# Kernel tuning notes

Measured on AMD Instinct MI355X. Metric: run time of the kernel, lower is better.

The kernel has to match this reference:

```python
import jax, jax.numpy as jnp
import numpy as np
from jax.scipy.special import erfinv

EMBED = 384
HEADS = 6
HEAD_DIM = EMBED // HEADS  # 64
N_FREQS = HEAD_DIM // 2    # 32
SEQ = 1025                 # 1 CLS + 32*32 patches
POS_DIM = 2
MIN_FREQ, MAX_FREQ = 0.1, 1000.0


def _phi(m: int) -> float:
    x = 2.0
    for _ in range(10):
        x = (1.0 + x) ** (1.0 / (m + 1.0))
    return x


def _uniform_directions(n: int, d: int) -> jnp.ndarray:
    # golden-ratio quasi-random directions, normalized (matches uniform_directions_jax)
    g = _phi(d)
    alpha = (1.0 / g) ** jnp.arange(1, d + 1, dtype=jnp.float32)
    i = jnp.arange(1, n + 1, dtype=jnp.float32)[:, None]
    z = jnp.fmod(i * alpha, 1.0)
    dirs = erfinv(2.0 * z - 1.0)
    return dirs / jnp.linalg.norm(dirs, axis=1, keepdims=True)


def _rope_freqs() -> jnp.ndarray:  # [h, F, P]
    omega = MIN_FREQ * (MAX_FREQ / MIN_FREQ) ** jnp.linspace(0.0, 1.0, N_FREQS)
    dirs = _uniform_directions(HEADS * N_FREQS, POS_DIM).reshape(HEADS, N_FREQS, POS_DIM)
    return dirs * omega.reshape(1, N_FREQS, 1)


def _coords_2d() -> jnp.ndarray:  # [S, 2], CLS at origin, patches in [-1,1]^2
    n = int(np.sqrt(SEQ - 1))  # 32
    yy, xx = jnp.meshgrid(jnp.arange(n), jnp.arange(n), indexing='ij')
    xf = xx.flatten().astype(jnp.float32) / (n - 1) * 2 - 1
    yf = yy.flatten().astype(jnp.float32) / (n - 1) * 2 - 1
    patch = jnp.stack([xf, yf], axis=1)
    return jnp.concatenate([jnp.zeros((1, 2), jnp.float32), patch], axis=0)


def _apply_rope(t_bshd, freqs_hFP, coords_SP):
    # theta: [S, h, F]
    theta = jnp.einsum('hfp,sp->shf', freqs_hFP, coords_SP)
    cos, sin = jnp.cos(theta), jnp.sin(theta)  # broadcast over batch
    x1, y1 = jnp.split(t_bshd, 2, axis=-1)     # [b,s,h,F] each
    return jnp.concatenate([x1 * cos - y1 * sin, x1 * sin + y1 * cos], axis=-1)


def setup_inputs() -> dict:
    key = jax.random.key(0)
    ks = jax.random.split(key, 6)
    scale = 1.0 / np.sqrt(EMBED)
    return {
        'x':  jax.random.normal(ks[0], (16, SEQ, EMBED), jnp.float32),
        'Wq': jax.random.normal(ks[1], (EMBED, EMBED), jnp.float32) * scale,
        'Wk': jax.random.normal(ks[2], (EMBED, EMBED), jnp.float32) * scale,
        'Wv': jax.random.normal(ks[3], (EMBED, EMBED), jnp.float32) * scale,
        'Wo': jax.random.normal(ks[4], (EMBED, EMBED), jnp.float32) * scale,
        'bo': jnp.zeros((EMBED,), jnp.float32),
    }


def reference(x, Wq, Wk, Wv, Wo, bo):
    b, s, e = x.shape
    freqs = _rope_freqs()   # constant buffers
    coords = _coords_2d()
    q = (x @ Wq).reshape(b, s, HEADS, HEAD_DIM)
    k = (x @ Wk).reshape(b, s, HEADS, HEAD_DIM)
    v = (x @ Wv).reshape(b, s, HEADS, HEAD_DIM)
    q = _apply_rope(q, freqs, coords)
    k = _apply_rope(k, freqs, coords)
    scores = jnp.einsum('blhd,bmhd->bhlm', q, k) / np.sqrt(HEAD_DIM)
    attn = jax.nn.softmax(scores, axis=-1)
    out = jnp.einsum('bhlm,bmhd->blhd', attn, v).reshape(b, s, e)
    return out @ Wo + bo
```

## Files before the change

kernel.cpp:

```cpp
#include <hip/hip_runtime.h>
#include <hip/hip_bf16.h>
#include <math.h>

#define EMBED 384
#define HEADS 6
#define HD    64
#define NF    32
#define SEQ   1025
#define SEQP  1088
#define BATCH 16
#define MTOT  (BATCH*SEQ)
#define NCHUNK 17
#define LSTRIDE 72
#define VSTR   68

#define NB_X2B 6150
#define NB_TW  144
#define NB_RT  769

typedef __bf16 bf16x8 __attribute__((ext_vector_type(8)));
typedef __bf16 bf16x4 __attribute__((ext_vector_type(4)));
typedef float  f32x4  __attribute__((ext_vector_type(4)));
typedef short  s16x4  __attribute__((ext_vector_type(4)));

#define MFMA_BF16(A,B,C) __builtin_amdgcn_mfma_f32_16x16x32_bf16((A),(B),(C),0,0,0)
#define MFMA16(A,B,C) __builtin_amdgcn_mfma_f32_16x16x16bf16_1k((A),(B),(C),0,0,0)

#define GLL16(gp, lp) __builtin_amdgcn_global_load_lds( \
    (const __attribute__((address_space(1))) void*)(gp), \
    (__attribute__((address_space(3))) void*)(lp), 16, 0, 0)

__device__ __forceinline__ __bf16 f2bf(float f){
    __hip_bfloat16 h = __float2bfloat16(f);
    return *reinterpret_cast<__bf16*>(&h);
}
__device__ __forceinline__ short bfbits(float f){
    __hip_bfloat16 h = __float2bfloat16(f);
    return *reinterpret_cast<short*>(&h);
}

__device__ __forceinline__ float erfinv_f(float x){
    float w = -log1pf(-x*x);
    float p;
    if (w < 5.0f){
        w -= 2.5f;
        p = 2.81022636e-08f;
        p = fmaf(p, w, 3.43273939e-07f);
        p = fmaf(p, w, -3.5233877e-06f);
        p = fmaf(p, w, -4.39150654e-06f);
        p = fmaf(p, w, 0.00021858087f);
        p = fmaf(p, w, -0.00125372503f);
        p = fmaf(p, w, -0.00417768164f);
        p = fmaf(p, w, 0.246640727f);
        p = fmaf(p, w, 1.50140941f);
    } else {
        w = sqrtf(w) - 3.0f;
        p = -0.000200214257f;
        p = fmaf(p, w, 0.000100950558f);
        p = fmaf(p, w, 0.00134934322f);
        p = fmaf(p, w, -0.00367342844f);
        p = fmaf(p, w, 0.00573950773f);
        p = fmaf(p, w, -0.0076224613f);
        p = fmaf(p, w, 0.00943887047f);
        p = fmaf(p, w, 1.00167406f);
        p = fmaf(p, w, 2.83297682f);
    }
    return p * x;
}

__global__ __launch_bounds__(256) void prep_kernel(
    const float* __restrict__ x, __hip_bfloat16* __restrict__ xb,
    const float* __restrict__ Wq, const float* __restrict__ Wk,
    const float* __restrict__ Wv, const float* __restrict__ Wo,
    __hip_bfloat16* __restrict__ Wt,
    float* __restrict__ cos_t, float* __restrict__ sin_t)
{
    __shared__ float tile[64][65];
    const int bid = blockIdx.x;
    const int tid = threadIdx.x;

    if (bid < NB_X2B){
        int i = bid*256 + tid;
        float4 v = *reinterpret_cast<const float4*>(x + (size_t)i*4);
        bf16x4 b; b[0]=f2bf(v.x); b[1]=f2bf(v.y); b[2]=f2bf(v.z); b[3]=f2bf(v.w);
        *reinterpret_cast<bf16x4*>(reinterpret_cast<__bf16*>(xb) + (size_t)i*4) = b;
        return;
    }
    if (bid < NB_X2B + NB_TW){
        int idx = bid - NB_X2B;
        const int mat = idx / 36;
        const int rem = idx % 36;
        const int kx = rem / 6, ny = rem % 6;
        const float* W = (mat==0)?Wq:(mat==1)?Wk:(mat==2)?Wv:Wo;
        const int k0 = kx*64, n0 = ny*64;
        const int c = tid & 63, rq = tid >> 6;
        #pragma unroll
        for (int i = 0; i < 16; ++i){
            int row = rq*16 + i;
            tile[row][c] = W[(size_t)(k0+row)*EMBED + n0 + c];
        }
        __syncthreads();
        #pragma unroll
        for (int i = 0; i < 16; ++i){
            int nr = rq*16 + i;
            Wt[((size_t)mat*EMBED + n0 + nr)*EMBED + k0 + c] = __float2bfloat16(tile[c][nr]);
        }
        return;
    }
    int idx = (bid - NB_X2B - NB_TW)*256 + tid;
    if (idx >= SEQ*HEADS*NF) return;
    int f  = idx & (NF-1);
    int hf = idx / NF;
    int h  = hf % HEADS;
    int s  = hf / HEADS;

    double xd = 2.0;
    #pragma unroll
    for (int it = 0; it < 10; ++it) xd = cbrt(1.0 + xd);
    float a1 = (float)(1.0 / xd);
    float a2 = a1 * a1;

    float fi = (float)(h*NF + f + 1);
    float z1 = fmodf(fi * a1, 1.0f);
    float z2 = fmodf(fi * a2, 1.0f);
    float d1 = erfinv_f(2.0f*z1 - 1.0f);
    float d2 = erfinv_f(2.0f*z2 - 1.0f);
    float inv = 1.0f / sqrtf(d1*d1 + d2*d2);
    d1 *= inv; d2 *= inv;

    float omega = 0.1f * powf(10000.0f, (float)f / 31.0f);
    float fx = d1 * omega, fy = d2 * omega;

    float cx = 0.0f, cy = 0.0f;
    if (s > 0){
        int pi = s - 1;
        cx = (float)(pi & 31) / 31.0f * 2.0f - 1.0f;
        cy = (float)(pi >> 5) / 31.0f * 2.0f - 1.0f;
    }
    float theta = fx*cx + fy*cy;
    float sv, cv;
    sincosf(theta, &sv, &cv);
    cos_t[idx] = cv;
    sin_t[idx] = sv;
}

__global__ __launch_bounds__(256, 3) void qkv_rope_kernel(
    const __hip_bfloat16* __restrict__ xb_,
    const __hip_bfloat16* __restrict__ Wt,
    const float* __restrict__ cos_t,
    const float* __restrict__ sin_t,
    __hip_bfloat16* __restrict__ qbuf,
    __hip_bfloat16* __restrict__ kbuf,
    __hip_bfloat16* __restrict__ vbuf)
{
    __shared__ __align__(16) __bf16 xs[2][128*32];
    __shared__ __align__(16) __bf16 bt[2][128*32];
    const int tid = threadIdx.x;
    const int m0 = blockIdx.x * 128;
    const int j  = blockIdx.y;
    const __bf16* xb = reinterpret_cast<const __bf16*>(xb_);
    const __bf16* wt = reinterpret_cast<const __bf16*>(Wt);

    const int w = tid >> 6;
    const int lane = tid & 63;
    const int quad = lane >> 4, low = lane & 15;
    const int rg = lane >> 2, cg = lane & 3;

    int arow[2], brow[2], loff[2];
    #pragma unroll
    for (int i = 0; i < 2; ++i){
        int row = (w*2 + i)*16 + rg;
        int am = m0 + row; if (am > MTOT-1) am = MTOT-1;
        arow[i] = am;
        brow[i] = j*128 + row;
        loff[i] = (w*2 + i)*1024;
    }

    #pragma unroll
    for (int i = 0; i < 2; ++i){
        GLL16(xb + (size_t)arow[i]*EMBED + cg*8, (char*)xs[0] + loff[i]);
        GLL16(wt + (size_t)brow[i]*EMBED + cg*8, (char*)bt[0] + loff[i]);
    }
    __syncthreads();

    const int mh = w >> 1, nh = w & 1;
    const int mw0 = m0 + mh*64;

    f32x4 acc[4][4] = {};
    for (int kb = 0; kb < 12; ++kb){
        const int cur = kb & 1;
        if (kb < 11){
            const int k1 = (kb+1)*32;
            #pragma unroll
            for (int i = 0; i < 2; ++i){
                GLL16(xb + (size_t)arow[i]*EMBED + k1 + cg*8, (char*)xs[cur^1] + loff[i]);
                GLL16(wt + (size_t)brow[i]*EMBED + k1 + cg*8, (char*)bt[cur^1] + loff[i]);
            }
        }
        bf16x8 af[4], bfr[4];
        #pragma unroll
        for (int mt = 0; mt < 4; ++mt)
            af[mt] = *reinterpret_cast<const bf16x8*>(&xs[cur][(mh*64 + mt*16 + low)*32 + quad*8]);
        #pragma unroll
        for (int t = 0; t < 4; ++t)
            bfr[t] = *reinterpret_cast<const bf16x8*>(&bt[cur][(nh*64 + t*16 + low)*32 + quad*8]);
        #pragma unroll
        for (int t = 0; t < 4; ++t)
            #pragma unroll
            for (int mt = 0; mt < 4; ++mt)
                acc[mt][t] = MFMA_BF16(af[mt], bfr[t], acc[mt][t]);
        if (kb < 11) __syncthreads();
    }

    const int n64 = j*2 + nh;
    const int mat = n64 / 6;
    const int h   = n64 % 6;

    if (mat == 2){
        #pragma unroll
        for (int mt = 0; mt < 4; ++mt)
            #pragma unroll
            for (int t = 0; t < 4; ++t)
                #pragma unroll
                for (int r = 0; r < 4; ++r){
                    int m = mw0 + mt*16 + quad*4 + r;
                    if (m < MTOT){
                        int b = m / SEQ, s = m % SEQ;
                        vbuf[((size_t)(b*HEADS + h)*SEQ + s)*HD + t*16 + low] = __float2bfloat16(acc[mt][t][r]);
                    }
                }
    } else {
        __hip_bfloat16* ob = (mat == 0) ? qbuf : kbuf;
        const float qs_ = (mat == 0) ? 0.125f : 1.0f;
        #pragma unroll
        for (int mt = 0; mt < 4; ++mt)
            #pragma unroll
            for (int t = 0; t < 2; ++t)
                #pragma unroll
                for (int r = 0; r < 4; ++r){
                    int m = mw0 + mt*16 + quad*4 + r;
                    if (m < MTOT){
                        int b = m / SEQ, s = m % SEQ;
                        int f = t*16 + low;
                        float cv = cos_t[(s*HEADS + h)*NF + f];
                        float sv = sin_t[(s*HEADS + h)*NF + f];
                        float x1 = acc[mt][t][r];
                        float y1 = acc[mt][t+2][r];
                        size_t base = ((size_t)(b*HEADS + h)*SEQ + s)*HD;
                        ob[base + f]      = __float2bfloat16((x1*cv - y1*sv)*qs_);
                        ob[base + NF + f] = __float2bfloat16((x1*sv + y1*cv)*qs_);
                    }
                }
    }
}

__global__ __launch_bounds__(256) void vt_transpose_kernel(
    const __hip_bfloat16* __restrict__ v, __hip_bfloat16* __restrict__ vt)
{
    __shared__ __bf16 tileT[64*72];
    const int tid = threadIdx.x;
    const int bh = blockIdx.x;
    const int s0 = blockIdx.y * 64;
    const __bf16* vb = reinterpret_cast<const __bf16*>(v) + (size_t)bh*SEQ*HD;
    #pragma unroll
    for (int i = 0; i < 2; ++i){
        int ch = tid + i*256;
        int srow = ch >> 3, dg = ch & 7;
        int s = s0 + srow; if (s > SEQ-1) s = SEQ-1;
        bf16x8 val = *reinterpret_cast<const bf16x8*>(vb + (size_t)s*HD + dg*8);
        #pragma unroll
        for (int e = 0; e < 8; ++e)
            tileT[(dg*8 + e)*72 + srow] = val[e];
    }
    __syncthreads();
    __bf16* ot = reinterpret_cast<__bf16*>(vt) + (size_t)bh*HD*SEQP;
    #pragma unroll
    for (int i = 0; i < 2; ++i){
        int ch = tid + i*256;
        int d = ch >> 3, sg = ch & 7;
        bf16x8 val = *reinterpret_cast<const bf16x8*>(&tileT[d*72 + sg*8]);
        *reinterpret_cast<bf16x8*>(ot + (size_t)d*SEQP + s0 + sg*8) = val;
    }
}

__global__ __launch_bounds__(256, 4) void attn_kernel(
    const __hip_bfloat16* __restrict__ qbuf,
    const __hip_bfloat16* __restrict__ kbuf,
    const __hip_bfloat16* __restrict__ vtbuf,
    __hip_bfloat16* __restrict__ aout)
{
    __shared__ __align__(16) __bf16 kls[64*LSTRIDE];
    __shared__ __align__(16) __bf16 vls[64*VSTR];
    const int tid  = threadIdx.x;
    const int w    = tid >> 6;
    const int lane = tid & 63;
    const int quad = lane >> 4, low = lane & 15;
    const int id = blockIdx.x;
    const int bh = id % 96;
    const int qt = id / 96;
    const int b = bh / HEADS, h = bh % HEADS;
    const __bf16* qb = reinterpret_cast<const __bf16*>(qbuf);
    const __bf16* kb = reinterpret_cast<const __bf16*>(kbuf);
    const __bf16* vt = reinterpret_cast<const __bf16*>(vtbuf);
    const size_t base   = (size_t)bh * SEQ * HD;
    const size_t vtbase = (size_t)bh * HD * SEQP;
    const int q0 = qt*128 + w*32;

    int srow[2], sgk[2], soffk[2], soffv[2];
    #pragma unroll
    for (int i = 0; i < 2; ++i){
        int ch = tid + i*256;
        srow[i] = ch >> 3; sgk[i] = ch & 7;
        soffk[i] = srow[i]*LSTRIDE + sgk[i]*8;
        soffv[i] = srow[i]*VSTR    + sgk[i]*8;
    }

    bf16x8 bq[2][2];
    #pragma unroll
    for (int nt = 0; nt < 2; ++nt){
        int qs = q0 + nt*16 + low; if (qs > SEQ-1) qs = SEQ-1;
        #pragma unroll
        for (int ks = 0; ks < 2; ++ks)
            bq[nt][ks] = *reinterpret_cast<const bf16x8*>(qb + base + (size_t)qs*HD + ks*32 + quad*8);
    }

    bf16x8 kr[2], vr[2];
    #pragma unroll
    for (int i = 0; i < 2; ++i){
        int kk = srow[i]; if (kk > SEQ-1) kk = SEQ-1;
        kr[i] = *reinterpret_cast<const bf16x8*>(kb + base + (size_t)kk*HD + sgk[i]*8);
        vr[i] = *reinterpret_cast<const bf16x8*>(vt + vtbase + (size_t)srow[i]*SEQP + sgk[i]*8);
    }

    f32x4 o[2][4] = {};
    float l_i[2] = {0.f, 0.f};

    for (int c = 0; c < NCHUNK; ++c){
        const int c0 = c*64;
        __syncthreads();
        #pragma unroll
        for (int i = 0; i < 2; ++i){
            *reinterpret_cast<bf16x8*>(&kls[soffk[i]]) = kr[i];
            bf16x4 vlo = __builtin_shufflevector(vr[i], vr[i], 0,1,2,3);
            bf16x4 vhi = __builtin_shufflevector(vr[i], vr[i], 4,5,6,7);
            *reinterpret_cast<bf16x4*>(&vls[soffv[i]])     = vlo;
            *reinterpret_cast<bf16x4*>(&vls[soffv[i] + 4]) = vhi;
        }
        __syncthreads();
        if (c + 1 < NCHUNK){
            const int c1 = c0 + 64;
            #pragma unroll
            for (int i = 0; i < 2; ++i){
                int kk = c1 + srow[i]; if (kk > SEQ-1) kk = SEQ-1;
                kr[i] = *reinterpret_cast<const bf16x8*>(kb + base + (size_t)kk*HD + sgk[i]*8);
                vr[i] = *reinterpret_cast<const bf16x8*>(vt + vtbase + (size_t)srow[i]*SEQP + c1 + sgk[i]*8);
            }
        }
        f32x4 st[4][2] = {};
        #pragma unroll
        for (int kt = 0; kt < 4; ++kt)
            #pragma unroll
            for (int ks = 0; ks < 2; ++ks){
                bf16x8 ak = *reinterpret_cast<const bf16x8*>(&kls[(kt*16 + low)*LSTRIDE + ks*32 + quad*8]);
                #pragma unroll
                for (int nt = 0; nt < 2; ++nt)
                    st[kt][nt] = MFMA_BF16(ak, bq[nt][ks], st[kt][nt]);
            }
        if (c0 + 64 > SEQ){
            #pragma unroll
            for (int kt = 0; kt < 4; ++kt)
                #pragma unroll
                for (int r = 0; r < 4; ++r){
                    int key = c0 + kt*16 + quad*4 + r;
                    if (key >= SEQ){ st[kt][0][r] = -1e30f; st[kt][1][r] = -1e30f; }
                }
        }
        s16x4 pa[4][2];
        #pragma unroll
        for (int nt = 0; nt < 2; ++nt)
            #pragma unroll
            for (int kt = 0; kt < 4; ++kt)
                #pragma unroll
                for (int r = 0; r < 4; ++r){
                    float p = __expf(st[kt][nt][r]);
                    l_i[nt] += p;
                    pa[kt][nt][r] = bfbits(p);
                }
        #pragma unroll
        for (int kt = 0; kt < 4; ++kt)
            #pragma unroll
            for (int dt = 0; dt < 4; ++dt){
                const s16x4 bv = *reinterpret_cast<const s16x4*>(&vls[(dt*16 + low)*VSTR + kt*16 + quad*4]);
                #pragma unroll
                for (int nt = 0; nt < 2; ++nt)
                    o[nt][dt] = MFMA16(pa[kt][nt], bv, o[nt][dt]);
            }
    }

    #pragma unroll
    for (int nt = 0; nt < 2; ++nt){
        l_i[nt] += __shfl_xor(l_i[nt], 16, 64);
        l_i[nt] += __shfl_xor(l_i[nt], 32, 64);
    }
    float lq[2][4];
    #pragma unroll
    for (int nt = 0; nt < 2; ++nt)
        #pragma unroll
        for (int r = 0; r < 4; ++r)
            lq[nt][r] = __shfl(l_i[nt], quad*4 + r, 64);

    #pragma unroll
    for (int nt = 0; nt < 2; ++nt)
        #pragma unroll
        for (int r = 0; r < 4; ++r){
            int s = q0 + nt*16 + quad*4 + r;
            if (s < SEQ){
                float inv = 1.0f / lq[nt][r];
                __hip_bfloat16* dst = aout + ((size_t)b*SEQ + s)*EMBED + h*HD;
                #pragma unroll
                for (int dt = 0; dt < 4; ++dt)
                    dst[dt*16 + low] = __float2bfloat16(o[nt][dt][r]*inv);
            }
        }
}

__global__ __launch_bounds__(128) void outproj_kernel(
    const __hip_bfloat16* __restrict__ a,
    const __hip_bfloat16* __restrict__ Wt,
    const float* __restrict__ bo,
    float* __restrict__ out)
{
    __shared__ __align__(16) __bf16 xs[2][64*32];
    __shared__ __align__(16) __bf16 bt[2][128*32];
    const int tid = threadIdx.x;
    const int m0 = blockIdx.x * 64;
    const int j  = blockIdx.y;
    const __bf16* ab = reinterpret_cast<const __bf16*>(a);
    const __bf16* wt = reinterpret_cast<const __bf16*>(Wt) + (size_t)3*EMBED*EMBED;

    const int w = tid >> 6;
    const int lane = tid & 63;
    const int quad = lane >> 4, low = lane & 15;
    const int rg = lane >> 2, cg = lane & 3;

    int arow[2], aoff[2];
    #pragma unroll
    for (int i = 0; i < 2; ++i){
        int row = (w*2 + i)*16 + rg;
        int am = m0 + row; if (am > MTOT-1) am = MTOT-1;
        arow[i] = am;
        aoff[i] = (w*2 + i)*1024;
    }
    int brow[4], boff[4];
    #pragma unroll
    for (int i = 0; i < 4; ++i){
        int row = (w*4 + i)*16 + rg;
        brow[i] = j*128 + row;
        boff[i] = (w*4 + i)*1024;
    }

    #pragma unroll
    for (int i = 0; i < 2; ++i)
        GLL16(ab + (size_t)arow[i]*EMBED + cg*8, (char*)xs[0] + aoff[i]);
    #pragma unroll
    for (int i = 0; i < 4; ++i)
        GLL16(wt + (size_t)brow[i]*EMBED + cg*8, (char*)bt[0] + boff[i]);
    __syncthreads();

    f32x4 acc[4][4] = {};
    for (int kb = 0; kb < 12; ++kb){
        const int cur = kb & 1;
        if (kb < 11){
            const int k1 = (kb+1)*32;
            #pragma unroll
            for (int i = 0; i < 2; ++i)
                GLL16(ab + (size_t)arow[i]*EMBED + k1 + cg*8, (char*)xs[cur^1] + aoff[i]);
            #pragma unroll
            for (int i = 0; i < 4; ++i)
                GLL16(wt + (size_t)brow[i]*EMBED + k1 + cg*8, (char*)bt[cur^1] + boff[i]);
        }
        bf16x8 af[4], bfr[4];
        #pragma unroll
        for (int mt = 0; mt < 4; ++mt)
            af[mt] = *reinterpret_cast<const bf16x8*>(&xs[cur][(mt*16 + low)*32 + quad*8]);
        #pragma unroll
        for (int t = 0; t < 4; ++t)
            bfr[t] = *reinterpret_cast<const bf16x8*>(&bt[cur][(w*64 + t*16 + low)*32 + quad*8]);
        #pragma unroll
        for (int t = 0; t < 4; ++t)
            #pragma unroll
            for (int mt = 0; mt < 4; ++mt)
                acc[mt][t] = MFMA_BF16(af[mt], bfr[t], acc[mt][t]);
        if (kb < 11) __syncthreads();
    }

    #pragma unroll
    for (int t = 0; t < 4; ++t){
        const int n = j*128 + w*64 + t*16 + low;
        const float bias = bo[n];
        #pragma unroll
        for (int mt = 0; mt < 4; ++mt)
            #pragma unroll
            for (int r = 0; r < 4; ++r){
                const int m = m0 + mt*16 + quad*4 + r;
                if (m < MTOT) out[(size_t)m*EMBED + n] = acc[mt][t][r] + bias;
            }
    }
}

extern "C" void kernel_launch(void* const* d_in, const int* in_sizes, int n_in,
                              void* d_out, int out_size, void* d_ws, size_t ws_size,
                              hipStream_t stream)
{
    const float* x  = (const float*)d_in[0];
    const float* Wq = (const float*)d_in[1];
    const float* Wk = (const float*)d_in[2];
    const float* Wv = (const float*)d_in[3];
    const float* Wo = (const float*)d_in[4];
    const float* bo = (const float*)d_in[5];
    float* out = (float*)d_out;

    const size_t NE = (size_t)MTOT * EMBED;
    const size_t VT = (size_t)BATCH*HEADS*HD*SEQP;
    char* ws = (char*)d_ws;
    size_t off = 0;
    __hip_bfloat16* qbuf = (__hip_bfloat16*)(ws + off); off += 2*NE;
    __hip_bfloat16* kbuf = (__hip_bfloat16*)(ws + off); off += 2*NE;
    __hip_bfloat16* abuf = (__hip_bfloat16*)(ws + off); off += 2*NE;
    __hip_bfloat16* vbuf = (__hip_bfloat16*)(ws + off); off += 2*NE;
    __hip_bfloat16* xbuf = (__hip_bfloat16*)(ws + off); off += 2*NE;
    __hip_bfloat16* vt   = (__hip_bfloat16*)(ws + off); off += 2*VT;
    __hip_bfloat16* Wt   = (__hip_bfloat16*)(ws + off); off += (size_t)4*EMBED*EMBED*2;
    float* cos_t = (float*)(ws + off); off += (size_t)SEQ*HEADS*NF*4;
    float* sin_t = (float*)(ws + off); off += (size_t)SEQ*HEADS*NF*4;

    prep_kernel<<<dim3(NB_X2B + NB_TW + NB_RT), dim3(256), 0, stream>>>(
        x, xbuf, Wq, Wk, Wv, Wo, Wt, cos_t, sin_t);
    qkv_rope_kernel<<<dim3((MTOT + 127)/128, 9), dim3(256), 0, stream>>>(xbuf, Wt, cos_t, sin_t, qbuf, kbuf, vbuf);
    vt_transpose_kernel<<<dim3(96, 17), dim3(256), 0, stream>>>(vbuf, vt);
    attn_kernel<<<dim3(864), dim3(256), 0, stream>>>(qbuf, kbuf, vt, abuf);
    outproj_kernel<<<dim3((MTOT + 63)/64, 3), dim3(128), 0, stream>>>(abuf, Wt, bo, out);
}
```

Before: 206.2 us.

## Fuse V transpose into QKV GEMM epilogue and drop separate transpose kernel

```diff
diff --git a/kernel.cpp b/kernel.cpp
--- a/kernel.cpp
+++ b/kernel.cpp
@@ -13,10 +13,12 @@
 #define NCHUNK 17
 #define LSTRIDE 72
 #define VSTR   68
+#define TSTR   66
 
 #define NB_X2B 6150
 #define NB_TW  144
 #define NB_RT  769
+#define NB_VF  192
 
 typedef __bf16 bf16x8 __attribute__((ext_vector_type(8)));
 typedef __bf16 bf16x4 __attribute__((ext_vector_type(4)));
@@ -73,7 +75,8 @@
     const float* __restrict__ Wq, const float* __restrict__ Wk,
     const float* __restrict__ Wv, const float* __restrict__ Wo,
     __hip_bfloat16* __restrict__ Wt,
-    float* __restrict__ cos_t, float* __restrict__ sin_t)
+    float* __restrict__ cos_t, float* __restrict__ sin_t,
+    __hip_bfloat16* __restrict__ vt)
 {
     __shared__ float tile[64][65];
     const int bid = blockIdx.x;
@@ -107,41 +110,51 @@
         }
         return;
     }
-    int idx = (bid - NB_X2B - NB_TW)*256 + tid;
-    if (idx >= SEQ*HEADS*NF) return;
-    int f  = idx & (NF-1);
-    int hf = idx / NF;
-    int h  = hf % HEADS;
-    int s  = hf / HEADS;
-
-    double xd = 2.0;
-    #pragma unroll
-    for (int it = 0; it < 10; ++it) xd = cbrt(1.0 + xd);
-    float a1 = (float)(1.0 / xd);
-    float a2 = a1 * a1;
-
-    float fi = (float)(h*NF + f + 1);
-    float z1 = fmodf(fi * a1, 1.0f);
-    float z2 = fmodf(fi * a2, 1.0f);
-    float d1 = erfinv_f(2.0f*z1 - 1.0f);
-    float d2 = erfinv_f(2.0f*z2 - 1.0f);
-    float inv = 1.0f / sqrtf(d1*d1 + d2*d2);
-    d1 *= inv; d2 *= inv;
-
-    float omega = 0.1f * powf(10000.0f, (float)f / 31.0f);
-    float fx = d1 * omega, fy = d2 * omega;
-
-    float cx = 0.0f, cy = 0.0f;
-    if (s > 0){
-        int pi = s - 1;
-        cx = (float)(pi & 31) / 31.0f * 2.0f - 1.0f;
-        cy = (float)(pi >> 5) / 31.0f * 2.0f - 1.0f;
-    }
-    float theta = fx*cx + fy*cy;
-    float sv, cv;
-    sincosf(theta, &sv, &cv);
-    cos_t[idx] = cv;
-    sin_t[idx] = sv;
+    if (bid < NB_X2B + NB_TW + NB_RT){
+        int idx = (bid - NB_X2B - NB_TW)*256 + tid;
+        if (idx >= SEQ*HEADS*NF) return;
+        int f  = idx & (NF-1);
+        int hf = idx / NF;
+        int h  = hf % HEADS;
+        int s  = hf / HEADS;
+
+        double xd = 2.0;
+        #pragma unroll
+        for (int it = 0; it < 10; ++it) xd = cbrt(1.0 + xd);
+        float a1 = (float)(1.0 / xd);
+        float a2 = a1 * a1;
+
+        float fi = (float)(h*NF + f + 1);
+        float z1 = fmodf(fi * a1, 1.0f);
+        float z2 = fmodf(fi * a2, 1.0f);
+        float d1 = erfinv_f(2.0f*z1 - 1.0f);
+        float d2 = erfinv_f(2.0f*z2 - 1.0f);
+        float inv = 1.0f / sqrtf(d1*d1 + d2*d2);
+        d1 *= inv; d2 *= inv;
+
+        float omega = 0.1f * powf(10000.0f, (float)f / 31.0f);
+        float fx = d1 * omega, fy = d2 * omega;
+
+        float cx = 0.0f, cy = 0.0f;
+        if (s > 0){
+            int pi = s - 1;
+            cx = (float)(pi & 31) / 31.0f * 2.0f - 1.0f;
+            cy = (float)(pi >> 5) / 31.0f * 2.0f - 1.0f;
+        }
+        float theta = fx*cx + fy*cy;
+        float sv, cv;
+        sincosf(theta, &sv, &cv);
+        cos_t[idx] = cv;
+        sin_t[idx] = sv;
+        return;
+    }
+    {
+        int g = (bid - NB_X2B - NB_TW - NB_RT)*256 + tid;
+        int row = g >> 3, sg = g & 7;
+        bf16x8 z = {};
+        *reinterpret_cast<bf16x8*>(reinterpret_cast<__bf16*>(vt)
+            + (size_t)row*SEQP + 1024 + sg*8) = z;
+    }
 }
 
 __global__ __launch_bounds__(256, 3) void qkv_rope_kernel(
@@ -151,15 +164,15 @@
     const float* __restrict__ sin_t,
     __hip_bfloat16* __restrict__ qbuf,
     __hip_bfloat16* __restrict__ kbuf,
-    __hip_bfloat16* __restrict__ vbuf)
+    __hip_bfloat16* __restrict__ vtbuf)
 {
-    __shared__ __align__(16) __bf16 xs[2][128*32];
-    __shared__ __align__(16) __bf16 bt[2][128*32];
+    __shared__ __align__(16) __bf16 smem[16384];
     const int tid = threadIdx.x;
     const int m0 = blockIdx.x * 128;
     const int j  = blockIdx.y;
     const __bf16* xb = reinterpret_cast<const __bf16*>(xb_);
     const __bf16* wt = reinterpret_cast<const __bf16*>(Wt);
+    __bf16* vtb = reinterpret_cast<__bf16*>(vtbuf);
 
     const int w = tid >> 6;
     const int lane = tid & 63;
@@ -178,8 +191,8 @@
 
     #pragma unroll
     for (int i = 0; i < 2; ++i){
-        GLL16(xb + (size_t)arow[i]*EMBED + cg*8, (char*)xs[0] + loff[i]);
-        GLL16(wt + (size_t)brow[i]*EMBED + cg*8, (char*)bt[0] + loff[i]);
+        GLL16(xb + (size_t)arow[i]*EMBED + cg*8, (char*)smem + loff[i]);
+        GLL16(wt + (size_t)brow[i]*EMBED + cg*8, (char*)(smem + 8192) + loff[i]);
     }
     __syncthreads();
 
@@ -189,21 +202,25 @@
     f32x4 acc[4][4] = {};
     for (int kb = 0; kb < 12; ++kb){
         const int cur = kb & 1;
+        __bf16* xcur = smem + cur*4096;
+        __bf16* bcur = smem + 8192 + cur*4096;
         if (kb < 11){
             const int k1 = (kb+1)*32;
+            __bf16* xnxt = smem + (cur^1)*4096;
+            __bf16* bnxt = smem + 8192 + (cur^1)*4096;
             #pragma unroll
             for (int i = 0; i < 2; ++i){
-                GLL16(xb + (size_t)arow[i]*EMBED + k1 + cg*8, (char*)xs[cur^1] + loff[i]);
-                GLL16(wt + (size_t)brow[i]*EMBED + k1 + cg*8, (char*)bt[cur^1] + loff[i]);
+                GLL16(xb + (size_t)arow[i]*EMBED + k1 + cg*8, (char*)xnxt + loff[i]);
+                GLL16(wt + (size_t)brow[i]*EMBED + k1 + cg*8, (char*)bnxt + loff[i]);
             }
         }
         bf16x8 af[4], bfr[4];
         #pragma unroll
         for (int mt = 0; mt < 4; ++mt)
-            af[mt] = *reinterpret_cast<const bf16x8*>(&xs[cur][(mh*64 + mt*16 + low)*32 + quad*8]);
+            af[mt] = *reinterpret_cast<const bf16x8*>(&xcur[(mh*64 + mt*16 + low)*32 + quad*8]);
         #pragma unroll
         for (int t = 0; t < 4; ++t)
-            bfr[t] = *reinterpret_cast<const bf16x8*>(&bt[cur][(nh*64 + t*16 + low)*32 + quad*8]);
+            bfr[t] = *reinterpret_cast<const bf16x8*>(&bcur[(nh*64 + t*16 + low)*32 + quad*8]);
         #pragma unroll
         for (int t = 0; t < 4; ++t)
             #pragma unroll
@@ -217,18 +234,51 @@
     const int h   = n64 % 6;
 
     if (mat == 2){
-        #pragma unroll
-        for (int mt = 0; mt < 4; ++mt)
-            #pragma unroll
-            for (int t = 0; t < 4; ++t)
-                #pragma unroll
-                for (int r = 0; r < 4; ++r){
-                    int m = mw0 + mt*16 + quad*4 + r;
-                    if (m < MTOT){
-                        int b = m / SEQ, s = m % SEQ;
-                        vbuf[((size_t)(b*HEADS + h)*SEQ + s)*HD + t*16 + low] = __float2bfloat16(acc[mt][t][r]);
+        __syncthreads();
+        const int d8 = lane >> 3, sg = lane & 7;
+        const int m0c = mw0 + sg*8;
+        const int b0 = m0c / SEQ;
+        const int s0 = m0c - b0*SEQ;
+        const bool fast = (m0c + 7 < MTOT) && (s0 + 7 < SEQ);
+        #pragma unroll
+        for (int ph = 0; ph < 2; ++ph){
+            if (mh == ph){
+                __bf16* tl = smem + nh*4608;
+                #pragma unroll
+                for (int mt = 0; mt < 4; ++mt)
+                    #pragma unroll
+                    for (int t = 0; t < 4; ++t)
+                        #pragma unroll
+                        for (int r = 0; r < 4; ++r)
+                            tl[(mt*16 + quad*4 + r)*TSTR + t*16 + low] = f2bf(acc[mt][t][r]);
+            }
+            __syncthreads();
+            if (mh == ph){
+                __bf16* tl = smem + nh*4608;
+                #pragma unroll
+                for (int db = 0; db < 8; ++db){
+                    const int d = db*8 + d8;
+                    if (fast){
+                        bf16x8 val;
+                        #pragma unroll
+                        for (int e = 0; e < 8; ++e) val[e] = tl[(sg*8+e)*TSTR + d];
+                        *reinterpret_cast<bf16x8*>(
+                            vtb + ((size_t)(b0*HEADS + h)*HD + d)*SEQP + s0) = val;
+                    } else {
+                        #pragma unroll
+                        for (int e = 0; e < 8; ++e){
+                            int m = m0c + e;
+                            if (m < MTOT){
+                                int bb = m / SEQ, ss = m - bb*SEQ;
+                                vtb[((size_t)(bb*HEADS + h)*HD + d)*SEQP + ss] =
+                                    tl[(sg*8+e)*TSTR + d];
+                            }
+                        }
                     }
                 }
+            }
+            __syncthreads();
+        }
     } else {
         __hip_bfloat16* ob = (mat == 0) ? qbuf : kbuf;
         const float qs_ = (mat == 0) ? 0.125f : 1.0f;
@@ -251,35 +301,6 @@
                         ob[base + NF + f] = __float2bfloat16((x1*sv + y1*cv)*qs_);
                     }
                 }
-    }
-}
-
-__global__ __launch_bounds__(256) void vt_transpose_kernel(
-    const __hip_bfloat16* __restrict__ v, __hip_bfloat16* __restrict__ vt)
-{
-    __shared__ __bf16 tileT[64*72];
-    const int tid = threadIdx.x;
-    const int bh = blockIdx.x;
-    const int s0 = blockIdx.y * 64;
-    const __bf16* vb = reinterpret_cast<const __bf16*>(v) + (size_t)bh*SEQ*HD;
-    #pragma unroll
-    for (int i = 0; i < 2; ++i){
-        int ch = tid + i*256;
-        int srow = ch >> 3, dg = ch & 7;
-        int s = s0 + srow; if (s > SEQ-1) s = SEQ-1;
-        bf16x8 val = *reinterpret_cast<const bf16x8*>(vb + (size_t)s*HD + dg*8);
-        #pragma unroll
-        for (int e = 0; e < 8; ++e)
-            tileT[(dg*8 + e)*72 + srow] = val[e];
-    }
-    __syncthreads();
-    __bf16* ot = reinterpret_cast<__bf16*>(vt) + (size_t)bh*HD*SEQP;
-    #pragma unroll
-    for (int i = 0; i < 2; ++i){
-        int ch = tid + i*256;
-        int d = ch >> 3, sg = ch & 7;
-        bf16x8 val = *reinterpret_cast<const bf16x8*>(&tileT[d*72 + sg*8]);
-        *reinterpret_cast<bf16x8*>(ot + (size_t)d*SEQP + s0 + sg*8) = val;
     }
 }
 
@@ -527,17 +548,15 @@
     __hip_bfloat16* qbuf = (__hip_bfloat16*)(ws + off); off += 2*NE;
     __hip_bfloat16* kbuf = (__hip_bfloat16*)(ws + off); off += 2*NE;
     __hip_bfloat16* abuf = (__hip_bfloat16*)(ws + off); off += 2*NE;
-    __hip_bfloat16* vbuf = (__hip_bfloat16*)(ws + off); off += 2*NE;
     __hip_bfloat16* xbuf = (__hip_bfloat16*)(ws + off); off += 2*NE;
     __hip_bfloat16* vt   = (__hip_bfloat16*)(ws + off); off += 2*VT;
     __hip_bfloat16* Wt   = (__hip_bfloat16*)(ws + off); off += (size_t)4*EMBED*EMBED*2;
     float* cos_t = (float*)(ws + off); off += (size_t)SEQ*HEADS*NF*4;
     float* sin_t = (float*)(ws + off); off += (size_t)SEQ*HEADS*NF*4;
 
-    prep_kernel<<<dim3(NB_X2B + NB_TW + NB_RT), dim3(256), 0, stream>>>(
-        x, xbuf, Wq, Wk, Wv, Wo, Wt, cos_t, sin_t);
-    qkv_rope_kernel<<<dim3((MTOT + 127)/128, 9), dim3(256), 0, stream>>>(xbuf, Wt, cos_t, sin_t, qbuf, kbuf, vbuf);
-    vt_transpose_kernel<<<dim3(96, 17), dim3(256), 0, stream>>>(vbuf, vt);
+    prep_kernel<<<dim3(NB_X2B + NB_TW + NB_RT + NB_VF), dim3(256), 0, stream>>>(
+        x, xbuf, Wq, Wk, Wv, Wo, Wt, cos_t, sin_t, vt);
+    qkv_rope_kernel<<<dim3((MTOT + 127)/128, 9), dim3(256), 0, stream>>>(xbuf, Wt, cos_t, sin_t, qbuf, kbuf, vt);
     attn_kernel<<<dim3(864), dim3(256), 0, stream>>>(qbuf, kbuf, vt, abuf);
     outproj_kernel<<<dim3((MTOT + 63)/64, 3), dim3(128), 0, stream>>>(abuf, Wt, bo, out);
 }
```

New measurement: 201.1 us. 2.5% less time.
